# Optimization experiments

Hardware: AMD Instinct MI355X
Metric: run time of the kernel (lower is better)

The kernel has to match this reference:

```python
import math
import jax, jax.numpy as jnp
import numpy as np

N_EMBD = 768
N_HEAD = 12
BLOCK_SIZE = 1024
B, T, N_ENC = 8, 1024, 257
EPS = 1e-5


def _ln(x, g, b):
    m = jnp.mean(x, axis=-1, keepdims=True)
    v = jnp.var(x, axis=-1, keepdims=True)
    return (x - m) * jax.lax.rsqrt(v + EPS) * g + b


def _heads(t, n_head):
    B_, N_, C_ = t.shape
    return t.reshape(B_, N_, n_head, C_ // n_head).transpose(0, 2, 1, 3)  # [B,H,N,D]


def setup_inputs() -> dict:
    key = jax.random.key(0)
    ks = jax.random.split(key, 16)
    s = 0.02
    d, h4, dq = N_EMBD, 4 * N_EMBD, N_EMBD // 4
    inp = {
        'x': jax.random.normal(ks[0], (B, T, d), jnp.float32),
        'x_enc': jax.random.normal(ks[1], (B, N_ENC, d), jnp.float32),
        'ln1_g': jnp.ones((d,), jnp.float32), 'ln1_b': jnp.zeros((d,), jnp.float32),
        'ln2_g': jnp.ones((d,), jnp.float32), 'ln2_b': jnp.zeros((d,), jnp.float32),
        'ln3_g': jnp.ones((d,), jnp.float32), 'ln3_b': jnp.zeros((d,), jnp.float32),
        'attn_w': jax.random.normal(ks[2], (d, 3 * d), jnp.float32) * s,
        'attn_bias': jnp.zeros((3 * d,), jnp.float32),
        'attn_proj_w': jax.random.normal(ks[3], (d, d), jnp.float32) * s,
        'attn_proj_b': jnp.zeros((d,), jnp.float32),
        'img_w': jax.random.normal(ks[4], (d, 2 * d), jnp.float32) * s,
        'img_b': jnp.zeros((2 * d,), jnp.float32),
        'cap_w': jax.random.normal(ks[5], (d, d), jnp.float32) * s,
        'cap_b': jnp.zeros((d,), jnp.float32),
        'cross_proj_w': jax.random.normal(ks[6], (d, d), jnp.float32) * s,
        'cross_proj_b': jnp.zeros((d,), jnp.float32),
        'ad1_w': jax.random.normal(ks[7], (d, dq), jnp.float32) * s,
        'ad1_b': jnp.zeros((dq,), jnp.float32),
        'ad2_w': jax.random.normal(ks[8], (dq, d), jnp.float32) * s,
        'ad2_b': jnp.zeros((d,), jnp.float32),
        'fc_w': jax.random.normal(ks[9], (d, h4), jnp.float32) * s,
        'fc_b': jnp.zeros((h4,), jnp.float32),
        'mproj_w': jax.random.normal(ks[10], (h4, d), jnp.float32) * s,
        'mproj_b': jnp.zeros((d,), jnp.float32),
    }
    return inp


def _block(x, x_enc, ln1_g, ln1_b, ln2_g, ln2_b, ln3_g, ln3_b,
           attn_w, attn_bias, attn_proj_w, attn_proj_b,
           img_w, img_b, cap_w, cap_b, cross_proj_w, cross_proj_b,
           ad1_w, ad1_b, ad2_w, ad2_b, fc_w, fc_b, mproj_w, mproj_b):
    d, nh = N_EMBD, N_HEAD
    hd = d // nh
    scale = 1.0 / math.sqrt(hd)

    def adapter(h):
        return jax.nn.relu(h @ ad1_w + ad1_b) @ ad2_w + ad2_b

    # --- causal self-attention ---
    h = _ln(x, ln1_g, ln1_b)
    qkv = h @ attn_w + attn_bias
    q, k, v = jnp.split(qkv, 3, axis=2)
    q, k, v = _heads(q, nh), _heads(k, nh), _heads(v, nh)  # [B,H,T,hd]
    att = jnp.einsum('bhqd,bhkd->bhqk', q, k) * scale
    Tq = x.shape[1]
    causal = jnp.tril(jnp.ones((Tq, Tq), bool))
    att = jnp.where(causal, att, -jnp.inf)
    att = jax.nn.softmax(att, axis=-1)
    sa = jnp.einsum('bhqk,bhkd->bhqd', att, v).transpose(0, 2, 1, 3).reshape(x.shape)
    sa = sa @ attn_proj_w + attn_proj_b
    x = x + adapter(sa)

    # --- cross-attention (queries from x, keys/values from x_enc) ---
    hq = _ln(x, ln1_g, ln1_b)
    he = _ln(x_enc, ln3_g, ln3_b)
    kv = he @ img_w + img_b
    k2, v2 = jnp.split(kv, 2, axis=2)
    q2 = hq @ cap_w + cap_b
    q2, k2, v2 = _heads(q2, nh), _heads(k2, nh), _heads(v2, nh)
    catt = jax.nn.softmax(jnp.einsum('bhqd,bhkd->bhqk', q2, k2) * scale, axis=-1)
    ca = jnp.einsum('bhqk,bhkd->bhqd', catt, v2).transpose(0, 2, 1, 3).reshape(x.shape)
    ca = ca @ cross_proj_w + cross_proj_b
    x = x + adapter(ca)

    # --- MLP ---
    hm = _ln(x, ln2_g, ln2_b)
    m = jax.nn.gelu(hm @ fc_w + fc_b, approximate=True) @ mproj_w + mproj_b
    x = x + adapter(m)
    return x, x_enc


def reference(x, x_enc, ln1_g, ln1_b, ln2_g, ln2_b, ln3_g, ln3_b,
              attn_w, attn_bias, attn_proj_w, attn_proj_b,
              img_w, img_b, cap_w, cap_b, cross_proj_w, cross_proj_b,
              ad1_w, ad1_b, ad2_w, ad2_b, fc_w, fc_b, mproj_w, mproj_b):
    return _block(x, x_enc, ln1_g, ln1_b, ln2_g, ln2_b, ln3_g, ln3_b,
                  attn_w, attn_bias, attn_proj_w, attn_proj_b,
                  img_w, img_b, cap_w, cap_b, cross_proj_w, cross_proj_b,
                  ad1_w, ad1_b, ad2_w, ad2_b, fc_w, fc_b, mproj_w, mproj_b)
```

## Files before the change

### kernel.cpp

```cpp
#include <hip/hip_runtime.h>

typedef unsigned short u16;
typedef short bf16x8 __attribute__((ext_vector_type(8)));
typedef float f32x4 __attribute__((ext_vector_type(4)));
typedef unsigned short u16x4 __attribute__((ext_vector_type(4)));

__device__ __forceinline__ u16 f2bf(float f) {
  union { float f; unsigned u; } v; v.f = f;
  unsigned u = v.u;
  unsigned r = (u + 0x7FFFu + ((u >> 16) & 1u)) >> 16;
  return (u16)r;
}
__device__ __forceinline__ float bf2f(u16 h) {
  union { unsigned u; float f; } v; v.u = ((unsigned)h) << 16;
  return v.f;
}
__device__ __forceinline__ unsigned cvt_pk_bf16(float lo, float hi) {
  unsigned d;
  asm("v_cvt_pk_bf16_f32 %0, %1, %2" : "=v"(d) : "v"(lo), "v"(hi));
  return d;
}
__device__ __forceinline__ float gelu_f(float x) {
  const float c1 = -2.302585093f;
  const float c2 = -0.1029620967f;
  float t = __builtin_fmaf(x * x, c2, c1) * x;
  float e = exp2f(t);
  return x * __builtin_amdgcn_rcpf(e + 1.0f);
}

#define GLD_LDS16(gp, lp)                                             \
  __builtin_amdgcn_global_load_lds(                                   \
      (const __attribute__((address_space(1))) void*)(gp),            \
      (__attribute__((address_space(3))) void*)(lp), 16, 0, 0)

template<int OFF>
__device__ __forceinline__ u16x4 tr16(unsigned a) {
  u16x4 d;
  asm volatile("ds_read_b64_tr_b16 %0, %1 offset:%2" : "=&v"(d) : "v"(a), "n"(OFF));
  return d;
}
__device__ __forceinline__ bf16x8 pack8(u16x4 a, u16x4 b) {
  union { u16x4 p[2]; bf16x8 v; } u;
  u.p[0] = a; u.p[1] = b;
  return u.v;
}
__device__ __forceinline__ u16x4 pack4(unsigned w0, unsigned w1) {
  union { unsigned w[2]; u16x4 v; } u;
  u.w[0] = w0; u.w[1] = w1;
  return u.v;
}

struct TrBatch {
  const float* W[9];
  u16* Bt[9];
  int K[9], N[9], Kpad[9], Npad[9];
  int tstart[10];
};
__global__ __launch_bounds__(256)
void transpose_all(TrBatch tb) {
  __shared__ float tile[64][65];
  const int tid = blockIdx.x;
  int mi = 0;
  while (mi < 8 && tid >= tb.tstart[mi + 1]) ++mi;
  const int lt = tid - tb.tstart[mi];
  const int tx = tb.Npad[mi] >> 6;
  const int n0 = (lt % tx) * 64;
  const int k0 = (lt / tx) * 64;
  const float* W = tb.W[mi];
  u16* Bt = tb.Bt[mi];
  const int K = tb.K[mi], N = tb.N[mi], Kpad = tb.Kpad[mi];
  const int t = threadIdx.x;
  const int c = t & 63;
  const int rb = t >> 6;
#pragma unroll
  for (int i = 0; i < 16; ++i) {
    int r = i * 4 + rb;
    float v = 0.f;
    if (k0 + r < K && n0 + c < N) v = W[(size_t)(k0 + r) * N + n0 + c];
    tile[r][c] = v;
  }
  __syncthreads();
#pragma unroll
  for (int i = 0; i < 16; ++i) {
    int r = i * 4 + rb;
    Bt[(size_t)(n0 + r) * Kpad + k0 + c] = f2bf(tile[c][r]);
  }
}

__global__ __launch_bounds__(64)
void ln_kernel(const float* __restrict__ X, const float* __restrict__ G,
               const float* __restrict__ Bv, u16* __restrict__ O, int Mreal) {
  const int row = blockIdx.x;
  const int l = threadIdx.x;
  u16* op = O + (size_t)row * 768;
  if (row >= Mreal) {
    u16x4 z = {0, 0, 0, 0};
#pragma unroll
    for (int i = 0; i < 3; ++i) *(u16x4*)(op + (i * 64 + l) * 4) = z;
    return;
  }
  const float* xp = X + (size_t)row * 768;
  float v[12];
  float s = 0.f, s2 = 0.f;
#pragma unroll
  for (int i = 0; i < 3; ++i) {
    float4 t4 = *(const float4*)(xp + (i * 64 + l) * 4);
    v[i * 4 + 0] = t4.x; v[i * 4 + 1] = t4.y; v[i * 4 + 2] = t4.z; v[i * 4 + 3] = t4.w;
    s += t4.x + t4.y + t4.z + t4.w;
    s2 += t4.x * t4.x + t4.y * t4.y + t4.z * t4.z + t4.w * t4.w;
  }
#pragma unroll
  for (int off = 32; off > 0; off >>= 1) {
    s += __shfl_xor(s, off);
    s2 += __shfl_xor(s2, off);
  }
  const float mean = s * (1.0f / 768.0f);
  const float var = s2 * (1.0f / 768.0f) - mean * mean;
  const float rstd = rsqrtf(var + 1e-5f);
#pragma unroll
  for (int i = 0; i < 3; ++i) {
    int base = (i * 64 + l) * 4;
    float4 g4 = *(const float4*)(G + base);
    float4 b4 = *(const float4*)(Bv + base);
    u16x4 o4;
    o4[0] = f2bf((v[i * 4 + 0] - mean) * rstd * g4.x + b4.x);
    o4[1] = f2bf((v[i * 4 + 1] - mean) * rstd * g4.y + b4.y);
    o4[2] = f2bf((v[i * 4 + 2] - mean) * rstd * g4.z + b4.z);
    o4[3] = f2bf((v[i * 4 + 3] - mean) * rstd * g4.w + b4.w);
    *(u16x4*)(op + base) = o4;
  }
}

template<bool DOLN, bool RESID>
__global__ __launch_bounds__(64)
void resid_ln(const float* __restrict__ S, float* __restrict__ D,
              const u16* __restrict__ P,
              const float* __restrict__ G, const float* __restrict__ Bv,
              u16* __restrict__ O) {
  const int row = blockIdx.x;
  const int l = threadIdx.x;
  const float* sp = S + (size_t)row * 768;
  float* dp = D + (size_t)row * 768;
  float v[12];
  float s = 0.f, s2 = 0.f;
#pragma unroll
  for (int i = 0; i < 3; ++i) {
    const int base = (i * 64 + l) * 4;
    float4 t4 = *(const float4*)(sp + base);
    if (RESID) {
      u16x4 p4 = *(const u16x4*)(P + (size_t)row * 768 + base);
      t4.x += bf2f(p4[0]); t4.y += bf2f(p4[1]);
      t4.z += bf2f(p4[2]); t4.w += bf2f(p4[3]);
    }
    v[i * 4 + 0] = t4.x; v[i * 4 + 1] = t4.y; v[i * 4 + 2] = t4.z; v[i * 4 + 3] = t4.w;
    s += t4.x + t4.y + t4.z + t4.w;
    s2 += t4.x * t4.x + t4.y * t4.y + t4.z * t4.z + t4.w * t4.w;
    *(float4*)(dp + base) = t4;
  }
  if (DOLN) {
#pragma unroll
    for (int off = 32; off > 0; off >>= 1) {
      s += __shfl_xor(s, off);
      s2 += __shfl_xor(s2, off);
    }
    const float mean = s * (1.0f / 768.0f);
    const float var = s2 * (1.0f / 768.0f) - mean * mean;
    const float rstd = rsqrtf(var + 1e-5f);
    u16* op = O + (size_t)row * 768;
#pragma unroll
    for (int i = 0; i < 3; ++i) {
      int base = (i * 64 + l) * 4;
      float4 g4 = *(const float4*)(G + base);
      float4 b4 = *(const float4*)(Bv + base);
      u16x4 o4;
      o4[0] = f2bf((v[i * 4 + 0] - mean) * rstd * g4.x + b4.x);
      o4[1] = f2bf((v[i * 4 + 1] - mean) * rstd * g4.y + b4.y);
      o4[2] = f2bf((v[i * 4 + 2] - mean) * rstd * g4.z + b4.z);
      o4[3] = f2bf((v[i * 4 + 3] - mean) * rstd * g4.w + b4.w);
      *(u16x4*)(op + base) = o4;
    }
  }
}

template<int MODE>
__global__ void gemm_bt(const u16* __restrict__ A, const u16* __restrict__ Bt,
                        void* __restrict__ C, const float* __restrict__ bias,
                        int K, int ldc, int nbias) {
  __shared__ u16 As[2 * 128 * 32];
  __shared__ u16 Bs[2 * 128 * 32];
  const int t = threadIdx.x;
  const int lane = t & 63;
  const int wid = t >> 6;
  const int wm = (wid >> 1) * 64;
  const int wn = (wid & 1) * 64;
  const int tm = blockIdx.x * 128;
  const int tn = blockIdx.y * 128;

  f32x4 zero = {0.f, 0.f, 0.f, 0.f};
  f32x4 acc[4][4];
#pragma unroll
  for (int i = 0; i < 4; ++i)
#pragma unroll
    for (int j = 0; j < 4; ++j) acc[i][j] = zero;

  const int rowA = lane & 15;
  const int kb = (((lane >> 4) ^ ((rowA >> 1) & 3)) << 3);
  const int kTiles = K >> 6;
  for (int kt = 0; kt < kTiles; ++kt) {
    const int kk = kt << 6;
#pragma unroll
    for (int i = 0; i < 4; ++i) {
      const int c = i * 256 + t;
      const int r = (c >> 2) & 127;
      const int cc = ((c >> 9) << 5) + ((((c & 3) ^ ((r >> 1) & 3))) << 3);
      GLD_LDS16(A + (size_t)(tm + r) * K + kk + cc, As + c * 8);
      GLD_LDS16(Bt + (size_t)(tn + r) * K + kk + cc, Bs + c * 8);
    }
    __syncthreads();
#pragma unroll
    for (int ks = 0; ks < 2; ++ks) {
      bf16x8 af[4], bfr[4];
      const int base = ks * 4096;
#pragma unroll
      for (int i = 0; i < 4; ++i) {
        af[i] = *(const bf16x8*)(As + base + (wm + i * 16 + rowA) * 32 + kb);
        bfr[i] = *(const bf16x8*)(Bs + base + (wn + i * 16 + rowA) * 32 + kb);
      }
#pragma unroll
      for (int mi = 0; mi < 4; ++mi)
#pragma unroll
        for (int ni = 0; ni < 4; ++ni)
          acc[mi][ni] = __builtin_amdgcn_mfma_f32_16x16x32_bf16(af[mi], bfr[ni], acc[mi][ni], 0, 0, 0);
    }
    __syncthreads();
  }
  const int col0 = lane & 15;
  const int row0 = (lane >> 4) << 2;
#pragma unroll
  for (int mi = 0; mi < 4; ++mi) {
#pragma unroll
    for (int ni = 0; ni < 4; ++ni) {
      int col = tn + wn + ni * 16 + col0;
      float bb = (col < nbias) ? bias[col] : 0.f;
      float vv[4];
#pragma unroll
      for (int r = 0; r < 4; ++r) {
        float v = acc[mi][ni][r] + bb;
        if (MODE == 1) v = fmaxf(v, 0.f);
        else if (MODE == 2) v = gelu_f(v);
        vv[r] = v;
      }
      unsigned w0 = cvt_pk_bf16(vv[0], vv[1]);
      unsigned w1 = cvt_pk_bf16(vv[2], vv[3]);
      size_t row = (size_t)(tm + wm + mi * 16 + row0);
      u16* cp = (u16*)C + row * ldc + col;
      cp[0] = (u16)w0;
      cp[(size_t)ldc] = (u16)(w0 >> 16);
      cp[(size_t)ldc * 2] = (u16)w1;
      cp[(size_t)ldc * 3] = (u16)(w1 >> 16);
    }
  }
}

template<int MODE>
__global__ __launch_bounds__(256)
void gemm_bt_m64(const u16* __restrict__ A, const u16* __restrict__ Bt,
                 void* __restrict__ C, const float* __restrict__ bias,
                 int K, int ldc, int nbias) {
  __shared__ u16 As[2 * 64 * 32];
  __shared__ u16 Bs[2 * 128 * 32];
  const int t = threadIdx.x;
  const int lane = t & 63;
  const int wid = t >> 6;
  const int wn = wid * 32;
  const int tm = blockIdx.x * 64;
  const int tn = blockIdx.y * 128;

  f32x4 zero = {0.f, 0.f, 0.f, 0.f};
  f32x4 acc[4][2];
#pragma unroll
  for (int i = 0; i < 4; ++i)
#pragma unroll
    for (int j = 0; j < 2; ++j) acc[i][j] = zero;

  const int rowA = lane & 15;
  const int kb = (((lane >> 4) ^ ((rowA >> 1) & 3)) << 3);
  const int kTiles = K >> 6;
  for (int kt = 0; kt < kTiles; ++kt) {
    const int kk = kt << 6;
#pragma unroll
    for (int i = 0; i < 2; ++i) {
      const int c = i * 256 + t;
      const int r = (c >> 2) & 63;
      const int cc = ((c >> 8) << 5) + ((((c & 3) ^ ((r >> 1) & 3))) << 3);
      GLD_LDS16(A + (size_t)(tm + r) * K + kk + cc, As + c * 8);
    }
#pragma unroll
    for (int i = 0; i < 4; ++i) {
      const int c = i * 256 + t;
      const int r = (c >> 2) & 127;
      const int cc = ((c >> 9) << 5) + ((((c & 3) ^ ((r >> 1) & 3))) << 3);
      GLD_LDS16(Bt + (size_t)(tn + r) * K + kk + cc, Bs + c * 8);
    }
    __syncthreads();
#pragma unroll
    for (int ks = 0; ks < 2; ++ks) {
      bf16x8 af[4], bfr[2];
#pragma unroll
      for (int i = 0; i < 4; ++i)
        af[i] = *(const bf16x8*)(As + ks * 2048 + (i * 16 + rowA) * 32 + kb);
#pragma unroll
      for (int j = 0; j < 2; ++j)
        bfr[j] = *(const bf16x8*)(Bs + ks * 4096 + (wn + j * 16 + rowA) * 32 + kb);
#pragma unroll
      for (int mi = 0; mi < 4; ++mi)
#pragma unroll
        for (int ni = 0; ni < 2; ++ni)
          acc[mi][ni] = __builtin_amdgcn_mfma_f32_16x16x32_bf16(af[mi], bfr[ni], acc[mi][ni], 0, 0, 0);
    }
    __syncthreads();
  }
  const int col0 = lane & 15;
  const int row0 = (lane >> 4) << 2;
#pragma unroll
  for (int mi = 0; mi < 4; ++mi) {
#pragma unroll
    for (int ni = 0; ni < 2; ++ni) {
      int col = tn + wn + ni * 16 + col0;
      float bb = (col < nbias) ? bias[col] : 0.f;
      float vv[4];
#pragma unroll
      for (int r = 0; r < 4; ++r) {
        float v = acc[mi][ni][r] + bb;
        if (MODE == 1) v = fmaxf(v, 0.f);
        vv[r] = v;
      }
      unsigned w0 = cvt_pk_bf16(vv[0], vv[1]);
      unsigned w1 = cvt_pk_bf16(vv[2], vv[3]);
      size_t row = (size_t)(tm + mi * 16 + row0);
      u16* cp = (u16*)C + row * ldc + col;
      cp[0] = (u16)w0;
      cp[(size_t)ldc] = (u16)(w0 >> 16);
      cp[(size_t)ldc * 2] = (u16)w1;
      cp[(size_t)ldc * 3] = (u16)(w1 >> 16);
    }
  }
}

struct GemmJob {
  const u16* A; const u16* Bt; u16* C; const float* bias;
  int K, ldc, nbias, mblocks;
};
__global__ __launch_bounds__(256)
void gemm_bt_dual(GemmJob j0, GemmJob j1, int split) {
  __shared__ u16 As[2 * 128 * 32];
  __shared__ u16 Bs[2 * 128 * 32];
  const int bid = blockIdx.x;
  const GemmJob& J = (bid < split) ? j0 : j1;
  const int lb = (bid < split) ? bid : bid - split;
  const int tm = (lb % J.mblocks) * 128;
  const int tn = (lb / J.mblocks) * 128;
  const u16* A = J.A;
  const u16* Bt = J.Bt;
  const int K = J.K;

  const int t = threadIdx.x;
  const int lane = t & 63;
  const int wid = t >> 6;
  const int wm = (wid >> 1) * 64;
  const int wn = (wid & 1) * 64;

  f32x4 zero = {0.f, 0.f, 0.f, 0.f};
  f32x4 acc[4][4];
#pragma unroll
  for (int i = 0; i < 4; ++i)
#pragma unroll
    for (int j = 0; j < 4; ++j) acc[i][j] = zero;

  const int rowA = lane & 15;
  const int kb = (((lane >> 4) ^ ((rowA >> 1) & 3)) << 3);
  const int kTiles = K >> 6;
  for (int kt = 0; kt < kTiles; ++kt) {
    const int kk = kt << 6;
#pragma unroll
    for (int i = 0; i < 4; ++i) {
      const int c = i * 256 + t;
      const int r = (c >> 2) & 127;
      const int cc = ((c >> 9) << 5) + ((((c & 3) ^ ((r >> 1) & 3))) << 3);
      GLD_LDS16(A + (size_t)(tm + r) * K + kk + cc, As + c * 8);
      GLD_LDS16(Bt + (size_t)(tn + r) * K + kk + cc, Bs + c * 8);
    }
    __syncthreads();
#pragma unroll
    for (int ks = 0; ks < 2; ++ks) {
      bf16x8 af[4], bfr[4];
      const int base = ks * 4096;
#pragma unroll
      for (int i = 0; i < 4; ++i) {
        af[i] = *(const bf16x8*)(As + base + (wm + i * 16 + rowA) * 32 + kb);
        bfr[i] = *(const bf16x8*)(Bs + base + (wn + i * 16 + rowA) * 32 + kb);
      }
#pragma unroll
      for (int mi = 0; mi < 4; ++mi)
#pragma unroll
        for (int ni = 0; ni < 4; ++ni)
          acc[mi][ni] = __builtin_amdgcn_mfma_f32_16x16x32_bf16(af[mi], bfr[ni], acc[mi][ni], 0, 0, 0);
    }
    __syncthreads();
  }
  const int col0 = lane & 15;
  const int row0 = (lane >> 4) << 2;
#pragma unroll
  for (int mi = 0; mi < 4; ++mi) {
#pragma unroll
    for (int ni = 0; ni < 4; ++ni) {
      int col = tn + wn + ni * 16 + col0;
      float bb = (col < J.nbias) ? J.bias[col] : 0.f;
      unsigned w0 = cvt_pk_bf16(acc[mi][ni][0] + bb, acc[mi][ni][1] + bb);
      unsigned w1 = cvt_pk_bf16(acc[mi][ni][2] + bb, acc[mi][ni][3] + bb);
      size_t row = (size_t)(tm + wm + mi * 16 + row0);
      u16* cp = J.C + row * J.ldc + col;
      cp[0] = (u16)w0;
      cp[(size_t)J.ldc] = (u16)(w0 >> 16);
      cp[(size_t)J.ldc * 2] = (u16)w1;
      cp[(size_t)J.ldc * 3] = (u16)(w1 >> 16);
    }
  }
}

template<bool CAUSAL>
__global__ __launch_bounds__(256)
void attn_mfma(const u16* __restrict__ Q, const u16* __restrict__ Kp,
               const u16* __restrict__ Vp, u16* __restrict__ O,
               int seqkv, int qrs, int krs,
               long long qBatch, long long kBatch,
               int qoff, int koff, int voff) {
  __shared__ __align__(16) u16 Ks[64 * 64];
  __shared__ __align__(16) u16 Vs[4096];
  __shared__ __align__(16) u16 Ps[4][1024];
  const int t = threadIdx.x;
  const int lane = t & 63;
  const int wid = t >> 6;
  const int b = blockIdx.x / 12, h = blockIdx.x % 12;
  const int yq = CAUSAL ? ((int)gridDim.y - 1 - (int)blockIdx.y) : (int)blockIdx.y;
  const int q0 = yq * 64;
  const int colid = lane & 15;
  const int rgrp = lane >> 4;

  const int kt_end = CAUSAL ? (yq + 1) : ((seqkv + 63) >> 6);

  const u16* qp = Q + (size_t)b * qBatch + qoff + (size_t)(q0 + wid * 16 + colid) * qrs + h * 64;
  bf16x8 qa[2];
#pragma unroll
  for (int s = 0; s < 2; ++s) qa[s] = *(const bf16x8*)(qp + s * 32 + (rgrp << 3));

  f32x4 oacc[4];
#pragma unroll
  for (int i = 0; i < 4; ++i) oacc[i] = (f32x4){0.f, 0.f, 0.f, 0.f};
  float m[4] = {-1e30f, -1e30f, -1e30f, -1e30f};
  float l[4] = {0.f, 0.f, 0.f, 0.f};

  const u16x4 one4 = {0x3F80, 0x3F80, 0x3F80, 0x3F80};
  const bf16x8 ones8 = pack8(one4, one4);

  const u16* kbase = Kp + (size_t)b * kBatch + koff + h * 64;
  const u16* vbase = Vp + (size_t)b * kBatch + voff + h * 64;

  const int srr = t >> 3, sdc = t & 7;
  int kwo[2], vwo[2];
#pragma unroll
  for (int i = 0; i < 2; ++i) {
    const int r = srr + 32 * i;
    kwo[i] = r * 64 + ((sdc ^ (r & 7)) << 3);
    vwo[i] = ((sdc >> 1) << 10) + (i << 9) + (((srr >> 2) & 1) << 8)
           + (((srr >> 3) & 3) << 6) + ((srr & 3) << 4) + (((2 * sdc) & 3) << 2);
  }
  const unsigned vs_base = (unsigned)(size_t)&Vs[0] + 8u * (unsigned)lane;
  const unsigned ps_base = (unsigned)(size_t)&Ps[wid][0] + 8u * (unsigned)lane;

  bf16x8 kz[2], vz[2];
  auto LOADT = [&](int kt) {
    const int k0 = kt * 64;
#pragma unroll
    for (int i = 0; i < 2; ++i) {
      const int tk = k0 + srr + 32 * i;
      const int dc = sdc << 3;
      kz[i] = (bf16x8){0, 0, 0, 0, 0, 0, 0, 0};
      vz[i] = (bf16x8){0, 0, 0, 0, 0, 0, 0, 0};
      if (tk < seqkv) {
        kz[i] = *(const bf16x8*)(kbase + (size_t)tk * krs + dc);
        vz[i] = *(const bf16x8*)(vbase + (size_t)tk * krs + dc);
      }
    }
  };
  LOADT(0);

  constexpr float SC2 = 0.18033688011112042f;

  for (int kt = 0; kt < kt_end; ++kt) {
    const int k0 = kt * 64;
#pragma unroll
    for (int i = 0; i < 2; ++i) {
      *(bf16x8*)&Ks[kwo[i]] = kz[i];
      *(bf16x8*)&Vs[vwo[i]] = vz[i];
    }
    __syncthreads();
    if (kt + 1 < kt_end) LOADT(kt + 1);

    f32x4 sacc[4];
#pragma unroll
    for (int c = 0; c < 4; ++c) sacc[c] = (f32x4){0.f, 0.f, 0.f, 0.f};
#pragma unroll
    for (int c = 0; c < 4; ++c)
#pragma unroll
      for (int s = 0; s < 2; ++s) {
        bf16x8 kf = *(const bf16x8*)&Ks[(c * 16 + colid) * 64 +
                                        ((((s << 2) + rgrp) ^ (colid & 7)) << 3)];
        sacc[c] = __builtin_amdgcn_mfma_f32_16x16x32_bf16(qa[s], kf, sacc[c], 0, 0, 0);
      }

    const bool domask = CAUSAL ? (kt == yq) : (kt == kt_end - 1);
    if (domask) {
#pragma unroll
      for (int c = 0; c < 4; ++c) {
        int kv = k0 + c * 16 + colid;
#pragma unroll
        for (int r = 0; r < 4; ++r) {
          int q = q0 + wid * 16 + rgrp * 4 + r;
          if ((CAUSAL && kv > q) || (!CAUSAL && kv >= seqkv)) sacc[c][r] = -1e30f;
        }
      }
    }

    float pms[4];
#pragma unroll
    for (int r = 0; r < 4; ++r) {
      float v = fmaxf(fmaxf(sacc[0][r], sacc[1][r]), fmaxf(sacc[2][r], sacc[3][r]));
#pragma unroll
      for (int off = 1; off < 16; off <<= 1) v = fmaxf(v, __shfl_xor(v, off));
      pms[r] = v * SC2;
    }
    bool ok = (pms[0] <= m[0] + 8.f) && (pms[1] <= m[1] + 8.f) &&
              (pms[2] <= m[2] + 8.f) && (pms[3] <= m[3] + 8.f);
    if (!__all(ok)) {
#pragma unroll
      for (int r = 0; r < 4; ++r) {
        float newm = fmaxf(m[r], pms[r]);
        float corr = exp2f(m[r] - newm);
        m[r] = newm;
        l[r] *= corr;
#pragma unroll
        for (int dc2 = 0; dc2 < 4; ++dc2) oacc[dc2][r] *= corr;
      }
    }

    float pv[4][4];
#pragma unroll
    for (int c = 0; c < 4; ++c)
#pragma unroll
      for (int r = 0; r < 4; ++r)
        pv[c][r] = exp2f(__builtin_fmaf(sacc[c][r], SC2, -m[r]));

#pragma unroll
    for (int c = 0; c < 4; ++c) {
      unsigned w0 = cvt_pk_bf16(pv[c][0], pv[c][1]);
      unsigned w1 = cvt_pk_bf16(pv[c][2], pv[c][3]);
      const int pa = ((c >> 1) << 9) + (((colid >> 2) & 1) << 8)
                   + (((2 * c + (colid >> 3)) & 3) << 6) + ((colid & 3) << 4) + (rgrp << 2);
      *(u16x4*)&Ps[wid][pa] = pack4(w0, w1);
    }
    __builtin_amdgcn_sched_barrier(0);

    u16x4 p00 = tr16<0>(ps_base);
    u16x4 p01 = tr16<512>(ps_base);
    u16x4 p10 = tr16<1024>(ps_base);
    u16x4 p11 = tr16<1536>(ps_base);
    asm volatile("s_waitcnt lgkmcnt(0)" ::: "memory");
    __builtin_amdgcn_sched_barrier(0);
    bf16x8 pf0 = pack8(p00, p01);
    bf16x8 pf1 = pack8(p10, p11);

    f32x4 sum_acc = (f32x4){0.f, 0.f, 0.f, 0.f};
    sum_acc = __builtin_amdgcn_mfma_f32_16x16x32_bf16(pf0, ones8, sum_acc, 0, 0, 0);
    sum_acc = __builtin_amdgcn_mfma_f32_16x16x32_bf16(pf1, ones8, sum_acc, 0, 0, 0);

#pragma unroll
    for (int dc2 = 0; dc2 < 4; ++dc2) {
      const unsigned va = vs_base + (unsigned)(dc2 * 2048);
      u16x4 v00 = tr16<0>(va);
      u16x4 v01 = tr16<512>(va);
      u16x4 v10 = tr16<1024>(va);
      u16x4 v11 = tr16<1536>(va);
      asm volatile("s_waitcnt lgkmcnt(0)" ::: "memory");
      __builtin_amdgcn_sched_barrier(0);
      bf16x8 vf0 = pack8(v00, v01);
      bf16x8 vf1 = pack8(v10, v11);
      oacc[dc2] = __builtin_amdgcn_mfma_f32_16x16x32_bf16(pf0, vf0, oacc[dc2], 0, 0, 0);
      oacc[dc2] = __builtin_amdgcn_mfma_f32_16x16x32_bf16(pf1, vf1, oacc[dc2], 0, 0, 0);
    }
#pragma unroll
    for (int r = 0; r < 4; ++r) l[r] += sum_acc[r];
    __syncthreads();
  }

#pragma unroll
  for (int r = 0; r < 4; ++r) {
    int qrow = q0 + wid * 16 + rgrp * 4 + r;
    u16* op = O + ((size_t)b * 1024 + qrow) * 768 + h * 64;
    float inv = 1.f / l[r];
    unsigned w0 = cvt_pk_bf16(oacc[0][r] * inv, oacc[1][r] * inv);
    unsigned w1 = cvt_pk_bf16(oacc[2][r] * inv, oacc[3][r] * inv);
    op[colid] = (u16)w0;
    op[16 + colid] = (u16)(w0 >> 16);
    op[32 + colid] = (u16)w1;
    op[48 + colid] = (u16)(w1 >> 16);
  }
}

extern "C" void kernel_launch(void* const* d_in, const int* in_sizes, int n_in,
                              void* d_out, int out_size, void* d_ws, size_t ws_size,
                              hipStream_t stream) {
  const float* x        = (const float*)d_in[0];
  const float* x_enc    = (const float*)d_in[1];
  const float* ln1_g    = (const float*)d_in[2];
  const float* ln1_b    = (const float*)d_in[3];
  const float* ln2_g    = (const float*)d_in[4];
  const float* ln2_b    = (const float*)d_in[5];
  const float* ln3_g    = (const float*)d_in[6];
  const float* ln3_b    = (const float*)d_in[7];
  const float* attn_w   = (const float*)d_in[8];
  const float* attn_bias= (const float*)d_in[9];
  const float* proj_w   = (const float*)d_in[10];
  const float* proj_b   = (const float*)d_in[11];
  const float* img_w    = (const float*)d_in[12];
  const float* img_b    = (const float*)d_in[13];
  const float* cap_w    = (const float*)d_in[14];
  const float* cap_b    = (const float*)d_in[15];
  const float* cross_w  = (const float*)d_in[16];
  const float* cross_b  = (const float*)d_in[17];
  const float* ad1_w    = (const float*)d_in[18];
  const float* ad1_b    = (const float*)d_in[19];
  const float* ad2_w    = (const float*)d_in[20];
  const float* ad2_b    = (const float*)d_in[21];
  const float* fc_w     = (const float*)d_in[22];
  const float* fc_b     = (const float*)d_in[23];
  const float* mproj_w  = (const float*)d_in[24];
  const float* mproj_b  = (const float*)d_in[25];

  const int Mx = 8192;
  const int Me = 2056;
  const int MeP = 2176;

  float* out_x  = (float*)d_out;
  float* out_xe = out_x + (size_t)Mx * 768;

  char* ws = (char*)d_ws;
  size_t off = 0;
  auto alloc = [&](size_t elems) {
    u16* p = (u16*)(ws + off);
    off = (off + elems * 2 + 255) & ~(size_t)255;
    return p;
  };
  u16* wt_attn  = alloc((size_t)2304 * 768);
  u16* wt_proj  = alloc((size_t)768 * 768);
  u16* wt_img   = alloc((size_t)1536 * 768);
  u16* wt_cap   = alloc((size_t)768 * 768);
  u16* wt_cross = alloc((size_t)768 * 768);
  u16* wt_ad1   = alloc((size_t)256 * 768);
  u16* wt_ad2   = alloc((size_t)768 * 256);
  u16* wt_fc    = alloc((size_t)3072 * 768);
  u16* wt_mproj = alloc((size_t)768 * 3072);
  u16* hbuf     = alloc((size_t)Mx * 768);
  u16* big      = alloc((size_t)Mx * 3072);
  u16* p0       = alloc((size_t)Mx * 768);
  u16* p1       = alloc((size_t)Mx * 768);
  u16* hid      = alloc((size_t)Mx * 256);
  u16* q2  = big;
  u16* kvb = big + (size_t)Mx * 768;

  hipMemcpyAsync(out_xe, x_enc, (size_t)Me * 768 * 4, hipMemcpyDeviceToDevice, stream);

  TrBatch tb;
  int nt = 0;
  tb.tstart[0] = 0;
  auto addT = [&](const float* W, u16* Bt, int K, int N, int Kp, int Np) {
    tb.W[nt] = W; tb.Bt[nt] = Bt; tb.K[nt] = K; tb.N[nt] = N;
    tb.Kpad[nt] = Kp; tb.Npad[nt] = Np;
    tb.tstart[nt + 1] = tb.tstart[nt] + (Np / 64) * (Kp / 64);
    ++nt;
  };
  addT(attn_w, wt_attn, 768, 2304, 768, 2304);
  addT(proj_w, wt_proj, 768, 768, 768, 768);
  addT(img_w, wt_img, 768, 1536, 768, 1536);
  addT(cap_w, wt_cap, 768, 768, 768, 768);
  addT(cross_w, wt_cross, 768, 768, 768, 768);
  addT(ad1_w, wt_ad1, 768, 192, 768, 256);
  addT(ad2_w, wt_ad2, 192, 768, 256, 768);
  addT(fc_w, wt_fc, 768, 3072, 768, 3072);
  addT(mproj_w, wt_mproj, 3072, 768, 3072, 768);
  transpose_all<<<tb.tstart[9], 256, 0, stream>>>(tb);

  auto GEMM = [&](const u16* A, const u16* Bt, void* C, const float* bias,
                  int M, int N, int K, int ldc, int nbias, int mode) {
    dim3 g(M / 128, N / 128);
    if (mode == 0)      gemm_bt<0><<<g, 256, 0, stream>>>(A, Bt, C, bias, K, ldc, nbias);
    else if (mode == 1) gemm_bt<1><<<g, 256, 0, stream>>>(A, Bt, C, bias, K, ldc, nbias);
    else                gemm_bt<2><<<g, 256, 0, stream>>>(A, Bt, C, bias, K, ldc, nbias);
  };
  auto GEMM_M64 = [&](const u16* A, const u16* Bt, void* C, const float* bias,
                      int M, int N, int K, int ldc, int nbias, int mode) {
    dim3 g(M / 64, N / 128);
    if (mode == 0) gemm_bt_m64<0><<<g, 256, 0, stream>>>(A, Bt, C, bias, K, ldc, nbias);
    else           gemm_bt_m64<1><<<g, 256, 0, stream>>>(A, Bt, C, bias, K, ldc, nbias);
  };
  auto ADAPTER = [&](const u16* in, u16* padw) {
    GEMM_M64(in, wt_ad1, hid, ad1_b, Mx, 256, 768, 256, 192, 1);
    GEMM_M64(hid, wt_ad2, padw, ad2_b, Mx, 768, 256, 768, 768, 0);
  };

  resid_ln<true, false><<<Mx, 64, 0, stream>>>(x, out_x, nullptr, ln1_g, ln1_b, hbuf);

  GEMM(hbuf, wt_attn, big, attn_bias, Mx, 2304, 768, 2304, 2304, 0);
  attn_mfma<true><<<dim3(96, 16), 256, 0, stream>>>(
      big, big, big, p0, 1024, 2304, 2304,
      (long long)1024 * 2304, (long long)1024 * 2304, 0, 768, 1536);
  GEMM_M64(p0, wt_proj, p1, proj_b, Mx, 768, 768, 768, 768, 0);
  ADAPTER(p1, p0);
  resid_ln<true, true><<<Mx, 64, 0, stream>>>(out_x, out_x, p0, ln1_g, ln1_b, hbuf);

  ln_kernel<<<MeP, 64, 0, stream>>>(x_enc, ln3_g, ln3_b, p0, Me);
  {
    GemmJob jkv = { p0,   wt_img, kvb, img_b, 768, 1536, 1536, MeP / 128 };
    GemmJob jq2 = { hbuf, wt_cap, q2,  cap_b, 768, 768,  768,  Mx / 128 };
    const int split = (MeP / 128) * (1536 / 128);
    const int total = split + (Mx / 128) * (768 / 128);
    gemm_bt_dual<<<total, 256, 0, stream>>>(jkv, jq2, split);
  }
  attn_mfma<false><<<dim3(96, 16), 256, 0, stream>>>(
      q2, kvb, kvb, p1, 257, 768, 1536,
      (long long)1024 * 768, (long long)257 * 1536, 0, 0, 768);
  GEMM_M64(p1, wt_cross, p0, cross_b, Mx, 768, 768, 768, 768, 0);
  ADAPTER(p0, p1);
  resid_ln<true, true><<<Mx, 64, 0, stream>>>(out_x, out_x, p1, ln2_g, ln2_b, hbuf);

  GEMM(hbuf, wt_fc, big, fc_b, Mx, 3072, 768, 3072, 3072, 2);
  GEMM_M64(big, wt_mproj, p0, mproj_b, Mx, 768, 3072, 768, 768, 0);
  ADAPTER(p0, p1);
  resid_ln<false, true><<<Mx, 64, 0, stream>>>(out_x, out_x, p1, nullptr, nullptr, nullptr);

  (void)in_sizes; (void)n_in; (void)out_size; (void)ws_size;
}
```

Baseline: 436.6 us.

## Use 128-query attention blocks and unpadded 64x64 tiles for adapter GEMMs

Both attention kernels now run 512-thread blocks covering 128 query rows, so each K/V tile staged in shared memory serves eight waves instead of four. Each thread loads one K/V row per tile, and the causal loop extends to 2*yq+2 tiles with masking on the last two. Separately, the adapter down-projection drops its padding from 256 to 192 columns and runs on a new 64x64-tile GEMM kernel; the up-projection uses K=192. The aim is less redundant K/V loading and no wasted padded adapter compute, at the cost of fewer attention blocks, coarser causal load balance, and masking on two tiles.

```diff
diff --git a/kernel.cpp b/kernel.cpp
--- a/kernel.cpp
+++ b/kernel.cpp
@@ -347,6 +347,75 @@
   }
 }
 
+template<int MODE>
+__global__ __launch_bounds__(256)
+void gemm_bt_6464(const u16* __restrict__ A, const u16* __restrict__ Bt,
+                  void* __restrict__ C, const float* __restrict__ bias,
+                  int K, int ldc, int nbias) {
+  __shared__ u16 As[2 * 64 * 32];
+  __shared__ u16 Bs[2 * 64 * 32];
+  const int t = threadIdx.x;
+  const int lane = t & 63;
+  const int wid = t >> 6;
+  const int wn = wid * 16;
+  const int tm = blockIdx.x * 64;
+  const int tn = blockIdx.y * 64;
+
+  f32x4 acc[4];
+#pragma unroll
+  for (int i = 0; i < 4; ++i) acc[i] = (f32x4){0.f, 0.f, 0.f, 0.f};
+
+  const int rowA = lane & 15;
+  const int kb = (((lane >> 4) ^ ((rowA >> 1) & 3)) << 3);
+  const int kTiles = K >> 6;
+  for (int kt = 0; kt < kTiles; ++kt) {
+    const int kk = kt << 6;
+#pragma unroll
+    for (int i = 0; i < 2; ++i) {
+      const int c = i * 256 + t;
+      const int r = (c >> 2) & 63;
+      const int cc = ((c >> 8) << 5) + ((((c & 3) ^ ((r >> 1) & 3))) << 3);
+      GLD_LDS16(A + (size_t)(tm + r) * K + kk + cc, As + c * 8);
+      GLD_LDS16(Bt + (size_t)(tn + r) * K + kk + cc, Bs + c * 8);
+    }
+    __syncthreads();
+#pragma unroll
+    for (int ks = 0; ks < 2; ++ks) {
+      bf16x8 af[4], bfr;
+#pragma unroll
+      for (int i = 0; i < 4; ++i)
+        af[i] = *(const bf16x8*)(As + ks * 2048 + (i * 16 + rowA) * 32 + kb);
+      bfr = *(const bf16x8*)(Bs + ks * 2048 + (wn + rowA) * 32 + kb);
+#pragma unroll
+      for (int mi = 0; mi < 4; ++mi)
+        acc[mi] = __builtin_amdgcn_mfma_f32_16x16x32_bf16(af[mi], bfr, acc[mi], 0, 0, 0);
+    }
+    __syncthreads();
+  }
+  const int col0 = lane & 15;
+  const int row0 = (lane >> 4) << 2;
+#pragma unroll
+  for (int mi = 0; mi < 4; ++mi) {
+    int col = tn + wn + col0;
+    float bb = (col < nbias) ? bias[col] : 0.f;
+    float vv[4];
+#pragma unroll
+    for (int r = 0; r < 4; ++r) {
+      float v = acc[mi][r] + bb;
+      if (MODE == 1) v = fmaxf(v, 0.f);
+      vv[r] = v;
+    }
+    unsigned w0 = cvt_pk_bf16(vv[0], vv[1]);
+    unsigned w1 = cvt_pk_bf16(vv[2], vv[3]);
+    size_t row = (size_t)(tm + mi * 16 + row0);
+    u16* cp = (u16*)C + row * ldc + col;
+    cp[0] = (u16)w0;
+    cp[(size_t)ldc] = (u16)(w0 >> 16);
+    cp[(size_t)ldc * 2] = (u16)w1;
+    cp[(size_t)ldc * 3] = (u16)(w1 >> 16);
+  }
+}
+
 struct GemmJob {
   const u16* A; const u16* Bt; u16* C; const float* bias;
   int K, ldc, nbias, mblocks;
@@ -429,7 +498,7 @@
 }
 
 template<bool CAUSAL>
-__global__ __launch_bounds__(256)
+__global__ __launch_bounds__(512)
 void attn_mfma(const u16* __restrict__ Q, const u16* __restrict__ Kp,
                const u16* __restrict__ Vp, u16* __restrict__ O,
                int seqkv, int qrs, int krs,
@@ -437,17 +506,17 @@
                int qoff, int koff, int voff) {
   __shared__ __align__(16) u16 Ks[64 * 64];
   __shared__ __align__(16) u16 Vs[4096];
-  __shared__ __align__(16) u16 Ps[4][1024];
+  __shared__ __align__(16) u16 Ps[8][1024];
   const int t = threadIdx.x;
   const int lane = t & 63;
   const int wid = t >> 6;
   const int b = blockIdx.x / 12, h = blockIdx.x % 12;
   const int yq = CAUSAL ? ((int)gridDim.y - 1 - (int)blockIdx.y) : (int)blockIdx.y;
-  const int q0 = yq * 64;
+  const int q0 = yq * 128;
   const int colid = lane & 15;
   const int rgrp = lane >> 4;
 
-  const int kt_end = CAUSAL ? (yq + 1) : ((seqkv + 63) >> 6);
+  const int kt_end = CAUSAL ? (2 * yq + 2) : ((seqkv + 63) >> 6);
 
   const u16* qp = Q + (size_t)b * qBatch + qoff + (size_t)(q0 + wid * 16 + colid) * qrs + h * 64;
   bf16x8 qa[2];
@@ -467,30 +536,21 @@
   const u16* vbase = Vp + (size_t)b * kBatch + voff + h * 64;
 
   const int srr = t >> 3, sdc = t & 7;
-  int kwo[2], vwo[2];
-#pragma unroll
-  for (int i = 0; i < 2; ++i) {
-    const int r = srr + 32 * i;
-    kwo[i] = r * 64 + ((sdc ^ (r & 7)) << 3);
-    vwo[i] = ((sdc >> 1) << 10) + (i << 9) + (((srr >> 2) & 1) << 8)
-           + (((srr >> 3) & 3) << 6) + ((srr & 3) << 4) + (((2 * sdc) & 3) << 2);
-  }
+  const int kwo = srr * 64 + ((sdc ^ (srr & 7)) << 3);
+  const int vwo = ((sdc >> 1) << 10) + ((srr >> 5) << 9) + (((srr >> 2) & 1) << 8)
+                + (((srr >> 3) & 3) << 6) + ((srr & 3) << 4) + (((2 * sdc) & 3) << 2);
   const unsigned vs_base = (unsigned)(size_t)&Vs[0] + 8u * (unsigned)lane;
   const unsigned ps_base = (unsigned)(size_t)&Ps[wid][0] + 8u * (unsigned)lane;
 
-  bf16x8 kz[2], vz[2];
+  bf16x8 kz, vz;
   auto LOADT = [&](int kt) {
-    const int k0 = kt * 64;
-#pragma unroll
-    for (int i = 0; i < 2; ++i) {
-      const int tk = k0 + srr + 32 * i;
-      const int dc = sdc << 3;
-      kz[i] = (bf16x8){0, 0, 0, 0, 0, 0, 0, 0};
-      vz[i] = (bf16x8){0, 0, 0, 0, 0, 0, 0, 0};
-      if (tk < seqkv) {
-        kz[i] = *(const bf16x8*)(kbase + (size_t)tk * krs + dc);
-        vz[i] = *(const bf16x8*)(vbase + (size_t)tk * krs + dc);
-      }
+    const int tk = kt * 64 + srr;
+    const int dc = sdc << 3;
+    kz = (bf16x8){0, 0, 0, 0, 0, 0, 0, 0};
+    vz = (bf16x8){0, 0, 0, 0, 0, 0, 0, 0};
+    if (tk < seqkv) {
+      kz = *(const bf16x8*)(kbase + (size_t)tk * krs + dc);
+      vz = *(const bf16x8*)(vbase + (size_t)tk * krs + dc);
     }
   };
   LOADT(0);
@@ -499,11 +559,8 @@
 
   for (int kt = 0; kt < kt_end; ++kt) {
     const int k0 = kt * 64;
-#pragma unroll
-    for (int i = 0; i < 2; ++i) {
-      *(bf16x8*)&Ks[kwo[i]] = kz[i];
-      *(bf16x8*)&Vs[vwo[i]] = vz[i];
-    }
+    *(bf16x8*)&Ks[kwo] = kz;
+    *(bf16x8*)&Vs[vwo] = vz;
     __syncthreads();
     if (kt + 1 < kt_end) LOADT(kt + 1);
 
@@ -519,7 +576,7 @@
         sacc[c] = __builtin_amdgcn_mfma_f32_16x16x32_bf16(qa[s], kf, sacc[c], 0, 0, 0);
       }
 
-    const bool domask = CAUSAL ? (kt == yq) : (kt == kt_end - 1);
+    const bool domask = CAUSAL ? (kt >= 2 * yq) : (kt == kt_end - 1);
     if (domask) {
 #pragma unroll
       for (int c = 0; c < 4; ++c) {
@@ -666,15 +723,15 @@
   u16* wt_img   = alloc((size_t)1536 * 768);
   u16* wt_cap   = alloc((size_t)768 * 768);
   u16* wt_cross = alloc((size_t)768 * 768);
-  u16* wt_ad1   = alloc((size_t)256 * 768);
-  u16* wt_ad2   = alloc((size_t)768 * 256);
+  u16* wt_ad1   = alloc((size_t)192 * 768);
+  u16* wt_ad2   = alloc((size_t)768 * 192);
   u16* wt_fc    = alloc((size_t)3072 * 768);
   u16* wt_mproj = alloc((size_t)768 * 3072);
   u16* hbuf     = alloc((size_t)Mx * 768);
   u16* big      = alloc((size_t)Mx * 3072);
   u16* p0       = alloc((size_t)Mx * 768);
   u16* p1       = alloc((size_t)Mx * 768);
-  u16* hid      = alloc((size_t)Mx * 256);
+  u16* hid      = alloc((size_t)Mx * 192);
   u16* q2  = big;
   u16* kvb = big + (size_t)Mx * 768;
 
@@ -694,8 +751,8 @@
   addT(img_w, wt_img, 768, 1536, 768, 1536);
   addT(cap_w, wt_cap, 768, 768, 768, 768);
   addT(cross_w, wt_cross, 768, 768, 768, 768);
-  addT(ad1_w, wt_ad1, 768, 192, 768, 256);
-  addT(ad2_w, wt_ad2, 192, 768, 256, 768);
+  addT(ad1_w, wt_ad1, 768, 192, 768, 192);
+  addT(ad2_w, wt_ad2, 192, 768, 192, 768);
   addT(fc_w, wt_fc, 768, 3072, 768, 3072);
   addT(mproj_w, wt_mproj, 3072, 768, 3072, 768);
   transpose_all<<<tb.tstart[9], 256, 0, stream>>>(tb);
@@ -714,14 +771,15 @@
     else           gemm_bt_m64<1><<<g, 256, 0, stream>>>(A, Bt, C, bias, K, ldc, nbias);
   };
   auto ADAPTER = [&](const u16* in, u16* padw) {
-    GEMM_M64(in, wt_ad1, hid, ad1_b, Mx, 256, 768, 256, 192, 1);
-    GEMM_M64(hid, wt_ad2, padw, ad2_b, Mx, 768, 256, 768, 768, 0);
+    dim3 g1(Mx / 64, 192 / 64);
+    gemm_bt_6464<1><<<g1, 256, 0, stream>>>(in, wt_ad1, hid, ad1_b, 768, 192, 192);
+    GEMM_M64(hid, wt_ad2, padw, ad2_b, Mx, 768, 192, 768, 768, 0);
   };
 
   resid_ln<true, false><<<Mx, 64, 0, stream>>>(x, out_x, nullptr, ln1_g, ln1_b, hbuf);
 
   GEMM(hbuf, wt_attn, big, attn_bias, Mx, 2304, 768, 2304, 2304, 0);
-  attn_mfma<true><<<dim3(96, 16), 256, 0, stream>>>(
+  attn_mfma<true><<<dim3(96, 8), 512, 0, stream>>>(
       big, big, big, p0, 1024, 2304, 2304,
       (long long)1024 * 2304, (long long)1024 * 2304, 0, 768, 1536);
   GEMM_M64(p0, wt_proj, p1, proj_b, Mx, 768, 768, 768, 768, 0);
@@ -736,7 +794,7 @@
     const int total = split + (Mx / 128) * (768 / 128);
     gemm_bt_dual<<<total, 256, 0, stream>>>(jkv, jq2, split);
   }
-  attn_mfma<false><<<dim3(96, 16), 256, 0, stream>>>(
+  attn_mfma<false><<<dim3(96, 8), 512, 0, stream>>>(
       q2, kvb, kvb, p1, 257, 768, 1536,
       (long long)1024 * 768, (long long)257 * 1536, 0, 0, 768);
   GEMM_M64(p1, wt_cross, p0, cross_b, Mx, 768, 768, 768, 768, 0);
```

Result: faster. 419.8 us, median of 2 (-3.8%).
